# Performance work log

Hardware: AMD Instinct MI355X
Metric: run time of the kernel (lower is better)

## Reference

```python
import jax, jax.numpy as jnp
import numpy as np
from jax import lax

BN_EPS = 1e-5


def _bn(t, g, b, m, v):
    # eval-mode BatchNorm2d over channel axis 1
    scale = (g / jnp.sqrt(v + BN_EPS))[None, :, None, None]
    return (t - m[None, :, None, None]) * scale + b[None, :, None, None]


def _conv1x1(t, w):
    # w: (out_c, in_c)
    return jnp.einsum('bchw,oc->bohw', t, w)


def setup_inputs() -> dict:
    key = jax.random.key(0)
    ks = jax.random.split(key, 8)
    B, C_in, H, W = 16, 640, 32, 32
    x = jax.random.normal(ks[0], (B, C_in, H, W), dtype=jnp.float32)

    def bn_params(k, c):
        k1, k2, k3, k4 = jax.random.split(k, 4)
        return (jax.random.normal(k1, (c,), jnp.float32) * 0.1 + 1.0,  # gamma
                jax.random.normal(k2, (c,), jnp.float32) * 0.1,        # beta
                jax.random.normal(k3, (c,), jnp.float32) * 0.1,        # running mean
                jax.random.uniform(k4, (c,), jnp.float32) + 0.5)       # running var

    bn1_g, bn1_b, bn1_m, bn1_v = bn_params(ks[1], 640)
    w_in = jax.random.normal(ks[2], (64, 640), jnp.float32) / np.sqrt(640)
    bnin_g, bnin_b, bnin_m, bnin_v = bn_params(ks[3], 64)
    w_emb = jax.random.normal(ks[4], (640, 1664), jnp.float32) / np.sqrt(1664)
    bne_g, bne_b, bne_m, bne_v = bn_params(ks[5], 640)
    w_out = jax.random.normal(ks[6], (640, 640), jnp.float32) / np.sqrt(640)
    bno_g, bno_b, bno_m, bno_v = bn_params(ks[7], 640)

    return dict(x=x,
                bn1_g=bn1_g, bn1_b=bn1_b, bn1_m=bn1_m, bn1_v=bn1_v,
                w_in=w_in, bnin_g=bnin_g, bnin_b=bnin_b, bnin_m=bnin_m, bnin_v=bnin_v,
                w_emb=w_emb, bne_g=bne_g, bne_b=bne_b, bne_m=bne_m, bne_v=bne_v,
                w_out=w_out, bno_g=bno_g, bno_b=bno_b, bno_m=bno_m, bno_v=bno_v)


def reference(x,
              bn1_g, bn1_b, bn1_m, bn1_v,
              w_in, bnin_g, bnin_b, bnin_m, bnin_v,
              w_emb, bne_g, bne_b, bne_m, bne_v,
              w_out, bno_g, bno_b, bno_m, bno_v):
    KH, KW = 5, 5
    x = jax.nn.relu(_bn(x, bn1_g, bn1_b, bn1_m, bn1_v))
    x = jax.nn.relu(_bn(_conv1x1(x, w_in), bnin_g, bnin_b, bnin_m, bnin_v))
    x0 = jax.nn.relu(x)  # second ReLU in original forward (no-op but faithful)
    # F.normalize(x, dim=1, p=2), eps=1e-12 (PyTorch default)
    norm = jnp.sqrt(jnp.sum(x0 * x0, axis=1, keepdims=True))
    identity = x0 / jnp.maximum(norm, 1e-12)
    b, c, h, w = identity.shape
    # unfold: (b, c*KH*KW, h, w), channel-major ordering matches torch Unfold
    patches = lax.conv_general_dilated_patches(
        identity, (KH, KW), (1, 1), ((2, 2), (2, 2)))
    corr = patches.reshape(b, c, KH * KW, h, w) * identity[:, :, None, :, :]
    corr = corr.reshape(b, c * KH * KW, h, w)
    # featureL2Norm: sqrt(sum(x^2, 1) + 1e-6)
    gs = corr / jnp.sqrt(jnp.sum(corr * corr, axis=1, keepdims=True) + 1e-6)
    feat = jnp.concatenate([identity, gs], axis=1)  # (b, 1664, h, w)
    e = jax.nn.relu(_bn(_conv1x1(feat, w_emb), bne_g, bne_b, bne_m, bne_v))
    out = _bn(_conv1x1(e, w_out), bno_g, bno_b, bno_m, bno_v)
    # dropout in eval mode = identity
    return out
```

## Files before the change

kernel.cpp:

```cpp
#include <hip/hip_runtime.h>
#include <math.h>

#define BN_EPS 1e-5f

using short8  = __attribute__((ext_vector_type(8))) short;
using f32x16  = __attribute__((ext_vector_type(16))) float;


__device__ __forceinline__ float bflo(unsigned u) { return __uint_as_float(u << 16); }
__device__ __forceinline__ float bfhi(unsigned u) { return __uint_as_float(u & 0xffff0000u); }

__device__ __forceinline__ unsigned bf16_rne(float f) {
    unsigned u = __float_as_uint(f);
    return (u + 0x7fffu + ((u >> 16) & 1u)) >> 16;
}
__device__ __forceinline__ unsigned pack_bf16(float lo, float hi) {
    return bf16_rne(lo) | (bf16_rne(hi) << 16);
}
__device__ __forceinline__ unsigned pk_hu(float lo, float hi) {
    unsigned a = __float_as_uint(lo) + 0x8000u;
    unsigned b = __float_as_uint(hi) + 0x8000u;
    return __builtin_amdgcn_perm(b, a, 0x07060302u);
}
__device__ __forceinline__ unsigned pmul_fast(unsigned a, unsigned b) {
    return pk_hu(bflo(a) * bflo(b), bfhi(a) * bfhi(b));
}

__global__ __launch_bounds__(256)
void k_prepAll(const float* __restrict__ g1, const float* __restrict__ b1,
               const float* __restrict__ m1, const float* __restrict__ v1,
               const float* __restrict__ w_in,
               const float* __restrict__ gi, const float* __restrict__ bi,
               const float* __restrict__ mi, const float* __restrict__ vi,
               const float* __restrict__ w_emb,
               const float* __restrict__ ge, const float* __restrict__ be,
               const float* __restrict__ me, const float* __restrict__ ve,
               const float* __restrict__ w_out,
               const float* __restrict__ go, const float* __restrict__ bo,
               const float* __restrict__ mo, const float* __restrict__ vo,
               float* __restrict__ s1, float* __restrict__ b1c,
               float* __restrict__ biasI, float* __restrict__ biasE, float* __restrict__ biasO,
               unsigned* __restrict__ wIt, unsigned* __restrict__ wEt, unsigned* __restrict__ wOt)
{
    __shared__ float row[1664];
    const int tid = threadIdx.x;

    if (blockIdx.x < 640) {
        const int oc = blockIdx.x;
#pragma unroll
        for (int it = 0; it < 2; it++) {
            int u = it * 256 + tid;
            if (u < 416)
                ((float4*)row)[u] = ((const float4*)&w_emb[(size_t)oc * 1664])[u];
        }
        __syncthreads();
        if (tid < 208) {
            int kc = tid >> 2, kh = (tid >> 1) & 1, ksub = tid & 1;
            int k0 = kc * 32 + kh * 16 + ksub * 8;
            float sc = ge[oc] * rsqrtf(ve[oc] + BN_EPS);
            float v[8];
#pragma unroll
            for (int j = 0; j < 8; j++) {
                int kgp = k0 + j;
                int orig;
                if (kgp < 64) orig = kgp;
                else { int t = kgp - 64; orig = 64 + (t & 63) * 25 + (t >> 6); }
                v[j] = row[orig] * sc;
            }
            int mt = oc >> 7, mf = (oc >> 5) & 3;
            int idx = (mt * 52 + kc) * 512 + (mf * 2 + kh) * 64 + ksub * 32 + (oc & 31);
            ((uint4*)wEt)[idx] = make_uint4(pack_bf16(v[0], v[1]), pack_bf16(v[2], v[3]),
                                            pack_bf16(v[4], v[5]), pack_bf16(v[6], v[7]));
        }
        return;
    }

    int i = (blockIdx.x - 640) * 256 + tid;

    if (i < 640) {
        float s = g1[i] * rsqrtf(v1[i] + BN_EPS);
        s1[i] = s; b1c[i] = b1[i] - m1[i] * s;
    } else if (i < 704) {
        int c = i - 640;
        float s = gi[c] * rsqrtf(vi[c] + BN_EPS);
        biasI[c] = bi[c] - mi[c] * s;
    } else if (i < 1344) {
        int c = i - 704;
        float s = ge[c] * rsqrtf(ve[c] + BN_EPS);
        biasE[c] = be[c] - me[c] * s;
    } else if (i < 1984) {
        int c = i - 1344;
        float s = go[c] * rsqrtf(vo[c] + BN_EPS);
        biasO[c] = bo[c] - mo[c] * s;
    }

    if (i >= 2048 && i < 7168) {
        int u = i - 2048;
        int kc = u >> 8, w = u & 255;
        int mf = w >> 7, kh = (w >> 6) & 1, sl = w & 63;
        int oc = mf * 32 + (sl & 31);
        int k0 = kc * 32 + kh * 16 + (sl >> 5) * 8;
        float sc = gi[oc] * rsqrtf(vi[oc] + BN_EPS);
        unsigned d[4];
#pragma unroll
        for (int q = 0; q < 4; q++)
            d[q] = pack_bf16(w_in[oc * 640 + k0 + 2 * q] * sc,
                             w_in[oc * 640 + k0 + 2 * q + 1] * sc);
        ((uint4*)wIt)[u] = make_uint4(d[0], d[1], d[2], d[3]);
    }

    if (i >= 8192 && i < 59392) {
        int u = i - 8192;
        int ci = u >> 9, w = u & 511;
        int mt = ci / 20, kc = ci - mt * 20;
        int mf = w >> 7, kh = (w >> 6) & 1, sl = w & 63;
        int oc = mt * 128 + mf * 32 + (sl & 31);
        int k0 = kc * 32 + kh * 16 + (sl >> 5) * 8;
        float sc = go[oc] * rsqrtf(vo[oc] + BN_EPS);
        unsigned d[4];
#pragma unroll
        for (int q = 0; q < 4; q++)
            d[q] = pack_bf16(w_out[oc * 640 + k0 + 2 * q] * sc,
                             w_out[oc * 640 + k0 + 2 * q + 1] * sc);
        ((uint4*)wOt)[u] = make_uint4(d[0], d[1], d[2], d[3]);
    }
}

__device__ __forceinline__ uint4 gen_feat_unit(const short* slab, const short* ctrs,
                                               int kcAbs, int t)
{
    const int hf = t >> 7, sl = t & 63;
    const int bkh = (t >> 6) & 1;
    const int cl = bkh * 16 + (sl >> 5) * 8;
    if (kcAbs < 2) {
        int spxC = (hf + 2) * 36 + (sl & 31) + 2;
        return *(const uint4*)&slab[spxC * 72 + kcAbs * 32 + cl];
    } else {
        int pxl = hf * 32 + (sl & 31);
        int idx = kcAbs - 2;
        int ksp = idx >> 1;
        int cb = (idx & 1) * 32 + cl;
        int kho = ksp / 5, kwo = ksp - kho * 5;
        int spx = (hf + kho) * 36 + (sl & 31) + kwo;
        const unsigned* nb = (const unsigned*)&slab[spx * 72 + cb];
        const unsigned* ct = (const unsigned*)&ctrs[pxl * 72 + cb];
        return make_uint4(pmul_fast(nb[0], ct[0]), pmul_fast(nb[1], ct[1]),
                          pmul_fast(nb[2], ct[2]), pmul_fast(nb[3], ct[3]));
    }
}

__global__ __launch_bounds__(640, 3)
void k_mega(const float* __restrict__ x,
            const float* __restrict__ s1, const float* __restrict__ b1c,
            const unsigned* __restrict__ wIt, const float* __restrict__ biasI,
            const unsigned* __restrict__ wEt, const float* __restrict__ biasE,
            const unsigned* __restrict__ wOt, const float* __restrict__ biasO,
            float* __restrict__ out)
{
    __shared__ short slab[216 * 72];
    __shared__ short ctrs[64 * 72];
    __shared__ float invDs[64];
    __shared__ char  stg[2][16384];
    __shared__ uint4 Ep[20 * 256];

    const int tid = threadIdx.x;
    const int l = tid & 63;
    const int w = tid >> 6;
    const int mt = w >> 1, mf0 = (w & 1) * 2;
    const int pt = blockIdx.x;
    const int b = pt >> 4, r0 = (pt & 15) * 2;

    if (w < 7) {
        const int spx = w * 32 + (l & 31);
        const int spxc = spx < 216 ? spx : 215;
        const int sr = spxc / 36, sc = spxc - sr * 36;
        const int r = r0 + sr - 2, cc = sc - 2;
        const bool valid = (spx < 216) && (r >= 0) && (r < 32) && (cc >= 0) && (cc < 32);
        const int rcl = min(max(r, 0), 31), ccl = min(max(cc, 0), 31);
        const float* xp = x + (size_t)b * 655360 + (size_t)(rcl * 32 + ccl);
        const float vm = valid ? 1.f : 0.f;

        f32x16 accI[2];
#pragma unroll
        for (int i = 0; i < 2; i++)
#pragma unroll
            for (int rr = 0; rr < 16; rr++) accI[i][rr] = 0.f;

        for (int kc = 0; kc < 20; kc++) {
            uint4 av[2][2];
#pragma unroll
            for (int mi2 = 0; mi2 < 2; mi2++)
#pragma unroll
                for (int kh = 0; kh < 2; kh++)
                    av[mi2][kh] = ((const uint4*)wIt)[kc * 256 + (mi2 << 7) + (kh << 6) + l];
#pragma unroll
            for (int kh = 0; kh < 2; kh++) {
                const int ch0 = kc * 32 + kh * 16 + (l >> 5) * 8;
                float4 sA = *(const float4*)&s1[ch0], sB = *(const float4*)&s1[ch0 + 4];
                float4 bA = *(const float4*)&b1c[ch0], bB = *(const float4*)&b1c[ch0 + 4];
                const float* xc = xp + (size_t)ch0 * 1024;
                float vv[8];
                vv[0] = fmaxf(fmaf(xc[0],    sA.x, bA.x), 0.f) * vm;
                vv[1] = fmaxf(fmaf(xc[1024], sA.y, bA.y), 0.f) * vm;
                vv[2] = fmaxf(fmaf(xc[2048], sA.z, bA.z), 0.f) * vm;
                vv[3] = fmaxf(fmaf(xc[3072], sA.w, bA.w), 0.f) * vm;
                vv[4] = fmaxf(fmaf(xc[4096], sB.x, bB.x), 0.f) * vm;
                vv[5] = fmaxf(fmaf(xc[5120], sB.y, bB.y), 0.f) * vm;
                vv[6] = fmaxf(fmaf(xc[6144], sB.z, bB.z), 0.f) * vm;
                vv[7] = fmaxf(fmaf(xc[7168], sB.w, bB.w), 0.f) * vm;
                unsigned bu[4] = { pack_bf16(vv[0], vv[1]), pack_bf16(vv[2], vv[3]),
                                   pack_bf16(vv[4], vv[5]), pack_bf16(vv[6], vv[7]) };
                short8 bf = *(short8*)bu;
                accI[0] = __builtin_amdgcn_mfma_f32_32x32x16_bf16(*(short8*)&av[0][kh], bf, accI[0], 0, 0, 0);
                accI[1] = __builtin_amdgcn_mfma_f32_32x32x16_bf16(*(short8*)&av[1][kh], bf, accI[1], 0, 0, 0);
            }
        }
        float ss = 0.f;
#pragma unroll
        for (int mi2 = 0; mi2 < 2; mi2++)
#pragma unroll
            for (int rg = 0; rg < 4; rg++) {
                float4 bb = *(const float4*)&biasI[mi2 * 32 + 8 * rg + 4 * (l >> 5)];
#pragma unroll
                for (int q = 0; q < 4; q++) {
                    float bv = (q == 0) ? bb.x : (q == 1) ? bb.y : (q == 2) ? bb.z : bb.w;
                    float t = fmaxf(accI[mi2][rg * 4 + q] + bv, 0.f);
                    accI[mi2][rg * 4 + q] = t;
                    ss = fmaf(t, t, ss);
                }
            }
        ss += __shfl_xor(ss, 32);
        float inv = 1.f / fmaxf(sqrtf(ss), 1e-12f);
        if (spx < 216) {
#pragma unroll
            for (int mi2 = 0; mi2 < 2; mi2++)
#pragma unroll
                for (int rg = 0; rg < 4; rg++) {
                    unsigned d0 = pack_bf16(accI[mi2][rg * 4 + 0] * inv, accI[mi2][rg * 4 + 1] * inv);
                    unsigned d1 = pack_bf16(accI[mi2][rg * 4 + 2] * inv, accI[mi2][rg * 4 + 3] * inv);
                    if (!valid) { d0 = 0u; d1 = 0u; }
                    *(uint2*)&slab[spx * 72 + mi2 * 32 + 8 * rg + 4 * (l >> 5)] = make_uint2(d0, d1);
                }
        }
    }
    __syncthreads();

    if (tid < 512) {
        int px = tid >> 3, part = tid & 7;
        int rh = px >> 5, rw = px & 31;
        float ctr[8];
        const unsigned* cp = (const unsigned*)&slab[((rh + 2) * 36 + rw + 2) * 72 + part * 8];
#pragma unroll
        for (int d = 0; d < 4; d++) { ctr[2 * d] = bflo(cp[d]); ctr[2 * d + 1] = bfhi(cp[d]); }
        float sum = 0.f;
#pragma unroll
        for (int k = 0; k < 25; k++) {
            const int kh = k / 5, kw = k % 5;
            const unsigned* nb = (const unsigned*)&slab[((rh + kh) * 36 + rw + kw) * 72 + part * 8];
#pragma unroll
            for (int d = 0; d < 4; d++) {
                float q0 = bflo(nb[d]) * ctr[2 * d];
                float q1 = bfhi(nb[d]) * ctr[2 * d + 1];
                sum = fmaf(q0, q0, sum); sum = fmaf(q1, q1, sum);
            }
        }
        sum += __shfl_xor(sum, 1);
        sum += __shfl_xor(sum, 2);
        sum += __shfl_xor(sum, 4);
        if (part == 0) invDs[px] = rsqrtf(sum + 1e-6f);
    }
    __syncthreads();

    if (tid < 512) {
        int px = tid >> 3, q = tid & 7;
        int spx = ((px >> 5) + 2) * 36 + (px & 31) + 2;
        const unsigned* src = (const unsigned*)&slab[spx * 72 + q * 8];
        float iv = invDs[px];
        unsigned d[4];
#pragma unroll
        for (int dd = 0; dd < 4; dd++)
            d[dd] = pk_hu(bflo(src[dd]) * iv, bfhi(src[dd]) * iv);
        *(uint4*)&ctrs[px * 72 + q * 8] = make_uint4(d[0], d[1], d[2], d[3]);
    }
    __syncthreads();

    const uint4* A = (const uint4*)wEt + (size_t)(mt * 52) * 512;
    const bool has2 = (tid < 384);

    f32x16 acc[2][2];
#pragma unroll
    for (int i = 0; i < 2; i++)
#pragma unroll
        for (int j = 0; j < 2; j++)
#pragma unroll
            for (int r = 0; r < 16; r++) acc[i][j][r] = 0.f;

    {
        uint4 f = gen_feat_unit(slab, ctrs, (tid >> 8), tid & 255);
        *(uint4*)&stg[0][tid * 16] = f;
        if (has2) {
            int u = tid + 640;
            uint4 f2 = gen_feat_unit(slab, ctrs, (u >> 8), u & 255);
            *(uint4*)&stg[0][u * 16] = f2;
        }
    }
    __syncthreads();

    for (int c = 0; c < 13; c++) {
        const int cur = c & 1, nxt = cur ^ 1;
        if (c < 12) {
            int kc0 = (c + 1) * 4;
            uint4 f = gen_feat_unit(slab, ctrs, kc0 + (tid >> 8), tid & 255);
            *(uint4*)&stg[nxt][tid * 16] = f;
            if (has2) {
                int u = tid + 640;
                uint4 f2 = gen_feat_unit(slab, ctrs, kc0 + (u >> 8), u & 255);
                *(uint4*)&stg[nxt][u * 16] = f2;
            }
        }
#pragma unroll
        for (int kcL = 0; kcL < 4; kcL++) {
            const int kc = c * 4 + kcL;
            uint4 av[2][2], bv[2][2];
#pragma unroll
            for (int mi = 0; mi < 2; mi++)
#pragma unroll
                for (int kh = 0; kh < 2; kh++)
                    av[mi][kh] = A[(size_t)kc * 512 + (((mf0 + mi) * 2 + kh) << 6) + l];
#pragma unroll
            for (int ni = 0; ni < 2; ni++)
#pragma unroll
                for (int kh = 0; kh < 2; kh++)
                    bv[ni][kh] = *(const uint4*)&stg[cur][(kcL * 256 + (ni << 7) + (kh << 6) + l) * 16];
#pragma unroll
            for (int kh = 0; kh < 2; kh++) {
                acc[0][0] = __builtin_amdgcn_mfma_f32_32x32x16_bf16(*(short8*)&av[0][kh], *(short8*)&bv[0][kh], acc[0][0], 0, 0, 0);
                acc[0][1] = __builtin_amdgcn_mfma_f32_32x32x16_bf16(*(short8*)&av[0][kh], *(short8*)&bv[1][kh], acc[0][1], 0, 0, 0);
                acc[1][0] = __builtin_amdgcn_mfma_f32_32x32x16_bf16(*(short8*)&av[1][kh], *(short8*)&bv[0][kh], acc[1][0], 0, 0, 0);
                acc[1][1] = __builtin_amdgcn_mfma_f32_32x32x16_bf16(*(short8*)&av[1][kh], *(short8*)&bv[1][kh], acc[1][1], 0, 0, 0);
            }
        }
        __syncthreads();
    }

#pragma unroll
    for (int mi = 0; mi < 2; mi++) {
        const int kbase = (w * 2 + mi) * 256;
#pragma unroll
        for (int ni = 0; ni < 2; ni++) {
#pragma unroll
            for (int rg = 0; rg < 4; rg++) {
                int ocb = w * 64 + mi * 32 + 8 * rg + 4 * (l >> 5);
                float4 bb = *(const float4*)&biasE[ocb];
                unsigned d0 = pack_bf16(fmaxf(acc[mi][ni][rg * 4 + 0] + bb.x, 0.f),
                                        fmaxf(acc[mi][ni][rg * 4 + 1] + bb.y, 0.f));
                unsigned d1 = pack_bf16(fmaxf(acc[mi][ni][rg * 4 + 2] + bb.z, 0.f),
                                        fmaxf(acc[mi][ni][rg * 4 + 3] + bb.w, 0.f));
                int unit = kbase + (ni << 7) + ((rg >> 1) << 6) + ((rg & 1) << 5) + (l & 31);
                ((uint2*)Ep)[unit * 2 + (l >> 5)] = make_uint2(d0, d1);
            }
        }
    }
    __syncthreads();

    const int p0 = pt * 64;
    const int hw0 = p0 & 1023;
    const uint4* Ao = (const uint4*)wOt + (size_t)(mt * 20) * 512;

    f32x16 acc2[2][2];
#pragma unroll
    for (int i = 0; i < 2; i++)
#pragma unroll
        for (int j = 0; j < 2; j++)
#pragma unroll
            for (int r = 0; r < 16; r++) acc2[i][j][r] = 0.f;

#pragma unroll 2
    for (int kc = 0; kc < 20; kc++) {
        uint4 av[2][2], bv[2][2];
#pragma unroll
        for (int mi = 0; mi < 2; mi++)
#pragma unroll
            for (int kh = 0; kh < 2; kh++)
                av[mi][kh] = Ao[(size_t)kc * 512 + (((mf0 + mi) * 2 + kh) << 6) + l];
#pragma unroll
        for (int ni = 0; ni < 2; ni++)
#pragma unroll
            for (int kh = 0; kh < 2; kh++)
                bv[ni][kh] = Ep[kc * 256 + (ni << 7) + (kh << 6) + l];
#pragma unroll
        for (int kh = 0; kh < 2; kh++) {
            acc2[0][0] = __builtin_amdgcn_mfma_f32_32x32x16_bf16(*(short8*)&av[0][kh], *(short8*)&bv[0][kh], acc2[0][0], 0, 0, 0);
            acc2[0][1] = __builtin_amdgcn_mfma_f32_32x32x16_bf16(*(short8*)&av[0][kh], *(short8*)&bv[1][kh], acc2[0][1], 0, 0, 0);
            acc2[1][0] = __builtin_amdgcn_mfma_f32_32x32x16_bf16(*(short8*)&av[1][kh], *(short8*)&bv[0][kh], acc2[1][0], 0, 0, 0);
            acc2[1][1] = __builtin_amdgcn_mfma_f32_32x32x16_bf16(*(short8*)&av[1][kh], *(short8*)&bv[1][kh], acc2[1][1], 0, 0, 0);
        }
    }

#pragma unroll
    for (int mi = 0; mi < 2; mi++)
#pragma unroll
        for (int ni = 0; ni < 2; ni++) {
            int pxl = ni * 32 + (l & 31);
#pragma unroll
            for (int r = 0; r < 16; r++) {
                int oc = w * 64 + mi * 32 + (r & 3) + 8 * (r >> 2) + 4 * (l >> 5);
                out[((size_t)b * 640 + oc) * 1024 + hw0 + pxl] = acc2[mi][ni][r] + biasO[oc];
            }
        }
}

extern "C" void kernel_launch(void* const* d_in, const int* in_sizes, int n_in,
                              void* d_out, int out_size, void* d_ws, size_t ws_size,
                              hipStream_t stream)
{
    const float* x    = (const float*)d_in[0];
    const float* g1   = (const float*)d_in[1];
    const float* b1   = (const float*)d_in[2];
    const float* m1   = (const float*)d_in[3];
    const float* v1   = (const float*)d_in[4];
    const float* w_in = (const float*)d_in[5];
    const float* gi   = (const float*)d_in[6];
    const float* bi   = (const float*)d_in[7];
    const float* mi   = (const float*)d_in[8];
    const float* vi   = (const float*)d_in[9];
    const float* w_emb= (const float*)d_in[10];
    const float* ge   = (const float*)d_in[11];
    const float* be   = (const float*)d_in[12];
    const float* me   = (const float*)d_in[13];
    const float* ve   = (const float*)d_in[14];
    const float* w_out= (const float*)d_in[15];
    const float* go   = (const float*)d_in[16];
    const float* bo   = (const float*)d_in[17];
    const float* mo   = (const float*)d_in[18];
    const float* vo   = (const float*)d_in[19];

    char* ws = (char*)d_ws;
    float*    s1    = (float*)(ws + 0);
    float*    b1c   = (float*)(ws + 2560);
    float*    biasI = (float*)(ws + 5120);
    float*    biasE = (float*)(ws + 5376);
    float*    biasO = (float*)(ws + 7936);
    unsigned* wIt   = (unsigned*)(ws + 16384);
    unsigned* wOt   = (unsigned*)(ws + 98304);
    unsigned* wEt   = (unsigned*)(ws + 917504);
    float*    out   = (float*)d_out;

    k_prepAll<<<872, 256, 0, stream>>>(g1, b1, m1, v1, w_in, gi, bi, mi, vi,
                                       w_emb, ge, be, me, ve, w_out, go, bo, mo, vo,
                                       s1, b1c, biasI, biasE, biasO, wIt, wEt, wOt);
    k_mega<<<256, 640, 0, stream>>>(x, s1, b1c, wIt, biasI,
                                    wEt, biasE, wOt, biasO, out);
}
```

Measured before the change: 196.2 us.

## Software-pipeline all three GEMM loops and alias LDS buffers into one arena

After: 194.0 us. No clear change (-1.2%).

```diff
diff --git a/kernel.cpp b/kernel.cpp
--- a/kernel.cpp
+++ b/kernel.cpp
@@ -157,11 +157,14 @@
             const unsigned* __restrict__ wOt, const float* __restrict__ biasO,
             float* __restrict__ out)
 {
-    __shared__ short slab[216 * 72];
-    __shared__ short ctrs[64 * 72];
-    __shared__ float invDs[64];
-    __shared__ char  stg[2][16384];
-    __shared__ uint4 Ep[20 * 256];
+    __shared__ __align__(16) char Lds[106112];
+    short* slab  = (short*)Lds;
+    float* s1L   = (float*)(Lds + 31104);
+    float* b1L   = (float*)(Lds + 31104 + 2560);
+    short* ctrs  = (short*)(Lds + 31104);
+    float* invDs = (float*)(Lds + 40320);
+    char*  stg   = Lds + 40576;
+    uint4* Ep    = (uint4*)Lds;
 
     const int tid = threadIdx.x;
     const int l = tid & 63;
@@ -169,6 +172,10 @@
     const int mt = w >> 1, mf0 = (w & 1) * 2;
     const int pt = blockIdx.x;
     const int b = pt >> 4, r0 = (pt & 15) * 2;
+
+    if (tid < 160)       ((float4*)s1L)[tid]       = ((const float4*)s1)[tid];
+    else if (tid < 320)  ((float4*)b1L)[tid - 160] = ((const float4*)b1c)[tid - 160];
+    __syncthreads();
 
     if (w < 7) {
         const int spx = w * 32 + (l & 31);
@@ -178,7 +185,7 @@
         const bool valid = (spx < 216) && (r >= 0) && (r < 32) && (cc >= 0) && (cc < 32);
         const int rcl = min(max(r, 0), 31), ccl = min(max(cc, 0), 31);
         const float* xp = x + (size_t)b * 655360 + (size_t)(rcl * 32 + ccl);
-        const float vm = valid ? 1.f : 0.f;
+        const int co = (l >> 5) * 8;
 
         f32x16 accI[2];
 #pragma unroll
@@ -186,33 +193,59 @@
 #pragma unroll
             for (int rr = 0; rr < 16; rr++) accI[i][rr] = 0.f;
 
+        float xv[16], xn[16];
+        uint4 av[2][2], avn[2][2];
+#pragma unroll
+        for (int kh = 0; kh < 2; kh++)
+#pragma unroll
+            for (int j = 0; j < 8; j++)
+                xv[kh * 8 + j] = xp[(size_t)(kh * 16 + co + j) * 1024];
+#pragma unroll
+        for (int mi2 = 0; mi2 < 2; mi2++)
+#pragma unroll
+            for (int kh = 0; kh < 2; kh++)
+                av[mi2][kh] = ((const uint4*)wIt)[(mi2 << 7) + (kh << 6) + l];
+
         for (int kc = 0; kc < 20; kc++) {
-            uint4 av[2][2];
-#pragma unroll
-            for (int mi2 = 0; mi2 < 2; mi2++)
+            if (kc < 19) {
 #pragma unroll
                 for (int kh = 0; kh < 2; kh++)
-                    av[mi2][kh] = ((const uint4*)wIt)[kc * 256 + (mi2 << 7) + (kh << 6) + l];
+#pragma unroll
+                    for (int j = 0; j < 8; j++)
+                        xn[kh * 8 + j] = xp[(size_t)((kc + 1) * 32 + kh * 16 + co + j) * 1024];
+#pragma unroll
+                for (int mi2 = 0; mi2 < 2; mi2++)
+#pragma unroll
+                    for (int kh = 0; kh < 2; kh++)
+                        avn[mi2][kh] = ((const uint4*)wIt)[(kc + 1) * 256 + (mi2 << 7) + (kh << 6) + l];
+            }
 #pragma unroll
             for (int kh = 0; kh < 2; kh++) {
-                const int ch0 = kc * 32 + kh * 16 + (l >> 5) * 8;
-                float4 sA = *(const float4*)&s1[ch0], sB = *(const float4*)&s1[ch0 + 4];
-                float4 bA = *(const float4*)&b1c[ch0], bB = *(const float4*)&b1c[ch0 + 4];
-                const float* xc = xp + (size_t)ch0 * 1024;
+                const int ch0 = kc * 32 + kh * 16 + co;
+                float4 sA = *(const float4*)&s1L[ch0], sB = *(const float4*)&s1L[ch0 + 4];
+                float4 bA = *(const float4*)&b1L[ch0], bB = *(const float4*)&b1L[ch0 + 4];
                 float vv[8];
-                vv[0] = fmaxf(fmaf(xc[0],    sA.x, bA.x), 0.f) * vm;
-                vv[1] = fmaxf(fmaf(xc[1024], sA.y, bA.y), 0.f) * vm;
-                vv[2] = fmaxf(fmaf(xc[2048], sA.z, bA.z), 0.f) * vm;
-                vv[3] = fmaxf(fmaf(xc[3072], sA.w, bA.w), 0.f) * vm;
-                vv[4] = fmaxf(fmaf(xc[4096], sB.x, bB.x), 0.f) * vm;
-                vv[5] = fmaxf(fmaf(xc[5120], sB.y, bB.y), 0.f) * vm;
-                vv[6] = fmaxf(fmaf(xc[6144], sB.z, bB.z), 0.f) * vm;
-                vv[7] = fmaxf(fmaf(xc[7168], sB.w, bB.w), 0.f) * vm;
+                vv[0] = fmaxf(fmaf(xv[kh * 8 + 0], sA.x, bA.x), 0.f);
+                vv[1] = fmaxf(fmaf(xv[kh * 8 + 1], sA.y, bA.y), 0.f);
+                vv[2] = fmaxf(fmaf(xv[kh * 8 + 2], sA.z, bA.z), 0.f);
+                vv[3] = fmaxf(fmaf(xv[kh * 8 + 3], sA.w, bA.w), 0.f);
+                vv[4] = fmaxf(fmaf(xv[kh * 8 + 4], sB.x, bB.x), 0.f);
+                vv[5] = fmaxf(fmaf(xv[kh * 8 + 5], sB.y, bB.y), 0.f);
+                vv[6] = fmaxf(fmaf(xv[kh * 8 + 6], sB.z, bB.z), 0.f);
+                vv[7] = fmaxf(fmaf(xv[kh * 8 + 7], sB.w, bB.w), 0.f);
                 unsigned bu[4] = { pack_bf16(vv[0], vv[1]), pack_bf16(vv[2], vv[3]),
                                    pack_bf16(vv[4], vv[5]), pack_bf16(vv[6], vv[7]) };
                 short8 bf = *(short8*)bu;
                 accI[0] = __builtin_amdgcn_mfma_f32_32x32x16_bf16(*(short8*)&av[0][kh], bf, accI[0], 0, 0, 0);
                 accI[1] = __builtin_amdgcn_mfma_f32_32x32x16_bf16(*(short8*)&av[1][kh], bf, accI[1], 0, 0, 0);
+            }
+            if (kc < 19) {
+#pragma unroll
+                for (int q = 0; q < 16; q++) xv[q] = xn[q];
+#pragma unroll
+                for (int mi2 = 0; mi2 < 2; mi2++)
+#pragma unroll
+                    for (int kh = 0; kh < 2; kh++) av[mi2][kh] = avn[mi2][kh];
             }
         }
         float ss = 0.f;
@@ -285,7 +318,6 @@
     __syncthreads();
 
     const uint4* A = (const uint4*)wEt + (size_t)(mt * 52) * 512;
-    const bool has2 = (tid < 384);
 
     f32x16 acc[2][2];
 #pragma unroll
@@ -295,53 +327,123 @@
 #pragma unroll
             for (int r = 0; r < 16; r++) acc[i][j][r] = 0.f;
 
-    {
-        uint4 f = gen_feat_unit(slab, ctrs, (tid >> 8), tid & 255);
-        *(uint4*)&stg[0][tid * 16] = f;
-        if (has2) {
-            int u = tid + 640;
-            uint4 f2 = gen_feat_unit(slab, ctrs, (u >> 8), u & 255);
-            *(uint4*)&stg[0][u * 16] = f2;
-        }
-    }
-    __syncthreads();
-
-    for (int c = 0; c < 13; c++) {
+    uint4 avc[2][2];
+#pragma unroll
+    for (int mi = 0; mi < 2; mi++)
+#pragma unroll
+        for (int kh = 0; kh < 2; kh++)
+            avc[mi][kh] = A[(((mf0 + mi) * 2 + kh) << 6) + l];
+
+#pragma unroll
+    for (int k = 0; k < 4; k++) {
+        int u = tid + k * 640;
+        if (u < 2048) {
+            uint4 f = gen_feat_unit(slab, ctrs, (u >> 8), u & 255);
+            *(uint4*)&stg[u * 16] = f;
+        }
+    }
+    __syncthreads();
+
+    uint4 bvc[2][2];
+#pragma unroll
+    for (int ni = 0; ni < 2; ni++)
+#pragma unroll
+        for (int kh = 0; kh < 2; kh++)
+            bvc[ni][kh] = *(const uint4*)&stg[((ni << 7) + (kh << 6) + l) * 16];
+
+#pragma unroll 1
+    for (int c = 0; c < 6; c++) {
         const int cur = c & 1, nxt = cur ^ 1;
-        if (c < 12) {
-            int kc0 = (c + 1) * 4;
-            uint4 f = gen_feat_unit(slab, ctrs, kc0 + (tid >> 8), tid & 255);
-            *(uint4*)&stg[nxt][tid * 16] = f;
-            if (has2) {
-                int u = tid + 640;
-                uint4 f2 = gen_feat_unit(slab, ctrs, kc0 + (u >> 8), u & 255);
-                *(uint4*)&stg[nxt][u * 16] = f2;
-            }
-        }
-#pragma unroll
-        for (int kcL = 0; kcL < 4; kcL++) {
-            const int kc = c * 4 + kcL;
-            uint4 av[2][2], bv[2][2];
+        const int base = c * 8;
+        {
+            const int nunits = (c < 5) ? 2048 : 1024;
+            const int nbase = base + 8;
+#pragma unroll
+            for (int k = 0; k < 4; k++) {
+                int u = tid + k * 640;
+                if (u < nunits) {
+                    uint4 f = gen_feat_unit(slab, ctrs, nbase + (u >> 8), u & 255);
+                    *(uint4*)&stg[nxt * 32768 + u * 16] = f;
+                }
+            }
+        }
+#pragma unroll
+        for (int kcL = 0; kcL < 8; kcL++) {
+            const int kc = base + kcL;
+            uint4 avn[2][2];
 #pragma unroll
             for (int mi = 0; mi < 2; mi++)
 #pragma unroll
                 for (int kh = 0; kh < 2; kh++)
-                    av[mi][kh] = A[(size_t)kc * 512 + (((mf0 + mi) * 2 + kh) << 6) + l];
+                    avn[mi][kh] = A[(size_t)(kc + 1) * 512 + (((mf0 + mi) * 2 + kh) << 6) + l];
+            uint4 bvn[2][2];
+            if (kcL < 7) {
+#pragma unroll
+                for (int ni = 0; ni < 2; ni++)
+#pragma unroll
+                    for (int kh = 0; kh < 2; kh++)
+                        bvn[ni][kh] = *(const uint4*)&stg[cur * 32768 + ((kcL + 1) * 256 + (ni << 7) + (kh << 6) + l) * 16];
+            }
+#pragma unroll
+            for (int kh = 0; kh < 2; kh++) {
+                acc[0][0] = __builtin_amdgcn_mfma_f32_32x32x16_bf16(*(short8*)&avc[0][kh], *(short8*)&bvc[0][kh], acc[0][0], 0, 0, 0);
+                acc[0][1] = __builtin_amdgcn_mfma_f32_32x32x16_bf16(*(short8*)&avc[0][kh], *(short8*)&bvc[1][kh], acc[0][1], 0, 0, 0);
+                acc[1][0] = __builtin_amdgcn_mfma_f32_32x32x16_bf16(*(short8*)&avc[1][kh], *(short8*)&bvc[0][kh], acc[1][0], 0, 0, 0);
+                acc[1][1] = __builtin_amdgcn_mfma_f32_32x32x16_bf16(*(short8*)&avc[1][kh], *(short8*)&bvc[1][kh], acc[1][1], 0, 0, 0);
+            }
+#pragma unroll
+            for (int mi = 0; mi < 2; mi++)
+#pragma unroll
+                for (int kh = 0; kh < 2; kh++) avc[mi][kh] = avn[mi][kh];
+            if (kcL < 7) {
+#pragma unroll
+                for (int ni = 0; ni < 2; ni++)
+#pragma unroll
+                    for (int kh = 0; kh < 2; kh++) bvc[ni][kh] = bvn[ni][kh];
+            }
+        }
+        __syncthreads();
+#pragma unroll
+        for (int ni = 0; ni < 2; ni++)
+#pragma unroll
+            for (int kh = 0; kh < 2; kh++)
+                bvc[ni][kh] = *(const uint4*)&stg[nxt * 32768 + ((ni << 7) + (kh << 6) + l) * 16];
+    }
+#pragma unroll
+    for (int kcL = 0; kcL < 4; kcL++) {
+        const int kc = 48 + kcL;
+        uint4 avn[2][2], bvn[2][2];
+        if (kcL < 3) {
+#pragma unroll
+            for (int mi = 0; mi < 2; mi++)
+#pragma unroll
+                for (int kh = 0; kh < 2; kh++)
+                    avn[mi][kh] = A[(size_t)(kc + 1) * 512 + (((mf0 + mi) * 2 + kh) << 6) + l];
 #pragma unroll
             for (int ni = 0; ni < 2; ni++)
 #pragma unroll
                 for (int kh = 0; kh < 2; kh++)
-                    bv[ni][kh] = *(const uint4*)&stg[cur][(kcL * 256 + (ni << 7) + (kh << 6) + l) * 16];
-#pragma unroll
-            for (int kh = 0; kh < 2; kh++) {
-                acc[0][0] = __builtin_amdgcn_mfma_f32_32x32x16_bf16(*(short8*)&av[0][kh], *(short8*)&bv[0][kh], acc[0][0], 0, 0, 0);
-                acc[0][1] = __builtin_amdgcn_mfma_f32_32x32x16_bf16(*(short8*)&av[0][kh], *(short8*)&bv[1][kh], acc[0][1], 0, 0, 0);
-                acc[1][0] = __builtin_amdgcn_mfma_f32_32x32x16_bf16(*(short8*)&av[1][kh], *(short8*)&bv[0][kh], acc[1][0], 0, 0, 0);
-                acc[1][1] = __builtin_amdgcn_mfma_f32_32x32x16_bf16(*(short8*)&av[1][kh], *(short8*)&bv[1][kh], acc[1][1], 0, 0, 0);
-            }
-        }
-        __syncthreads();
-    }
+                    bvn[ni][kh] = *(const uint4*)&stg[((kcL + 1) * 256 + (ni << 7) + (kh << 6) + l) * 16];
+        }
+#pragma unroll
+        for (int kh = 0; kh < 2; kh++) {
+            acc[0][0] = __builtin_amdgcn_mfma_f32_32x32x16_bf16(*(short8*)&avc[0][kh], *(short8*)&bvc[0][kh], acc[0][0], 0, 0, 0);
+            acc[0][1] = __builtin_amdgcn_mfma_f32_32x32x16_bf16(*(short8*)&avc[0][kh], *(short8*)&bvc[1][kh], acc[0][1], 0, 0, 0);
+            acc[1][0] = __builtin_amdgcn_mfma_f32_32x32x16_bf16(*(short8*)&avc[1][kh], *(short8*)&bvc[0][kh], acc[1][0], 0, 0, 0);
+            acc[1][1] = __builtin_amdgcn_mfma_f32_32x32x16_bf16(*(short8*)&avc[1][kh], *(short8*)&bvc[1][kh], acc[1][1], 0, 0, 0);
+        }
+        if (kcL < 3) {
+#pragma unroll
+            for (int mi = 0; mi < 2; mi++)
+#pragma unroll
+                for (int kh = 0; kh < 2; kh++) avc[mi][kh] = avn[mi][kh];
+#pragma unroll
+            for (int ni = 0; ni < 2; ni++)
+#pragma unroll
+                for (int kh = 0; kh < 2; kh++) bvc[ni][kh] = bvn[ni][kh];
+        }
+    }
+    __syncthreads();
 
 #pragma unroll
     for (int mi = 0; mi < 2; mi++) {
@@ -375,25 +477,49 @@
 #pragma unroll
             for (int r = 0; r < 16; r++) acc2[i][j][r] = 0.f;
 
-#pragma unroll 2
+    uint4 aoc[2][2], boc[2][2];
+#pragma unroll
+    for (int mi = 0; mi < 2; mi++)
+#pragma unroll
+        for (int kh = 0; kh < 2; kh++)
+            aoc[mi][kh] = Ao[(((mf0 + mi) * 2 + kh) << 6) + l];
+#pragma unroll
+    for (int ni = 0; ni < 2; ni++)
+#pragma unroll
+        for (int kh = 0; kh < 2; kh++)
+            boc[ni][kh] = Ep[(ni << 7) + (kh << 6) + l];
+
+#pragma unroll 4
     for (int kc = 0; kc < 20; kc++) {
-        uint4 av[2][2], bv[2][2];
-#pragma unroll
-        for (int mi = 0; mi < 2; mi++)
-#pragma unroll
-            for (int kh = 0; kh < 2; kh++)
-                av[mi][kh] = Ao[(size_t)kc * 512 + (((mf0 + mi) * 2 + kh) << 6) + l];
-#pragma unroll
-        for (int ni = 0; ni < 2; ni++)
-#pragma unroll
-            for (int kh = 0; kh < 2; kh++)
-                bv[ni][kh] = Ep[kc * 256 + (ni << 7) + (kh << 6) + l];
+        uint4 aon[2][2], bon[2][2];
+        if (kc < 19) {
+#pragma unroll
+            for (int mi = 0; mi < 2; mi++)
+#pragma unroll
+                for (int kh = 0; kh < 2; kh++)
+                    aon[mi][kh] = Ao[(size_t)(kc + 1) * 512 + (((mf0 + mi) * 2 + kh) << 6) + l];
+#pragma unroll
+            for (int ni = 0; ni < 2; ni++)
+#pragma unroll
+                for (int kh = 0; kh < 2; kh++)
+                    bon[ni][kh] = Ep[(kc + 1) * 256 + (ni << 7) + (kh << 6) + l];
+        }
 #pragma unroll
         for (int kh = 0; kh < 2; kh++) {
-            acc2[0][0] = __builtin_amdgcn_mfma_f32_32x32x16_bf16(*(short8*)&av[0][kh], *(short8*)&bv[0][kh], acc2[0][0], 0, 0, 0);
-            acc2[0][1] = __builtin_amdgcn_mfma_f32_32x32x16_bf16(*(short8*)&av[0][kh], *(short8*)&bv[1][kh], acc2[0][1], 0, 0, 0);
-            acc2[1][0] = __builtin_amdgcn_mfma_f32_32x32x16_bf16(*(short8*)&av[1][kh], *(short8*)&bv[0][kh], acc2[1][0], 0, 0, 0);
-            acc2[1][1] = __builtin_amdgcn_mfma_f32_32x32x16_bf16(*(short8*)&av[1][kh], *(short8*)&bv[1][kh], acc2[1][1], 0, 0, 0);
+            acc2[0][0] = __builtin_amdgcn_mfma_f32_32x32x16_bf16(*(short8*)&aoc[0][kh], *(short8*)&boc[0][kh], acc2[0][0], 0, 0, 0);
+            acc2[0][1] = __builtin_amdgcn_mfma_f32_32x32x16_bf16(*(short8*)&aoc[0][kh], *(short8*)&boc[1][kh], acc2[0][1], 0, 0, 0);
+            acc2[1][0] = __builtin_amdgcn_mfma_f32_32x32x16_bf16(*(short8*)&aoc[1][kh], *(short8*)&boc[0][kh], acc2[1][0], 0, 0, 0);
+            acc2[1][1] = __builtin_amdgcn_mfma_f32_32x32x16_bf16(*(short8*)&aoc[1][kh], *(short8*)&boc[1][kh], acc2[1][1], 0, 0, 0);
+        }
+        if (kc < 19) {
+#pragma unroll
+            for (int mi = 0; mi < 2; mi++)
+#pragma unroll
+                for (int kh = 0; kh < 2; kh++) aoc[mi][kh] = aon[mi][kh];
+#pragma unroll
+            for (int ni = 0; ni < 2; ni++)
+#pragma unroll
+                for (int kh = 0; kh < 2; kh++) boc[ni][kh] = bon[ni][kh];
         }
     }
 
```
